# Performance work log

Hardware: AMD Instinct MI355X
Metric: run time of the kernel (lower is better)

The kernel has to match this reference:

```python
import jax, jax.numpy as jnp
import numpy as np

N_HEADS = 16
MAX_CACHE_LEN = 8192
LN_EPS = 1e-5


def _layernorm(x, g, b):
    mu = jnp.mean(x, axis=-1, keepdims=True)
    var = jnp.var(x, axis=-1, keepdims=True)
    return (x - mu) * jax.lax.rsqrt(var + LN_EPS) * g + b


def setup_inputs() -> dict:
    key = jax.random.key(0)
    ks = jax.random.split(key, 8)
    b, t, d, latdim, past = 2, 2048, 2048, 512, 2048
    s = 0.02
    return {
        "x": jax.random.normal(ks[0], (b, t, d), jnp.float32),
        "latent_prev": jax.random.normal(ks[1], (b, past, latdim), jnp.float32),
        "Wq": jax.random.normal(ks[2], (d, d), jnp.float32) * s,
        "Wdown": jax.random.normal(ks[3], (d, latdim), jnp.float32) * s,
        "Wk_up": jax.random.normal(ks[4], (latdim, d), jnp.float32) * s,
        "Wv_up": jax.random.normal(ks[5], (latdim, d), jnp.float32) * s,
        "ln_g": jnp.ones((latdim,), jnp.float32),
        "ln_b": jnp.zeros((latdim,), jnp.float32),
        "Wo": jax.random.normal(ks[6], (d, d), jnp.float32) * s,
    }


def reference(x, latent_prev, Wq, Wdown, Wk_up, Wv_up, ln_g, ln_b, Wo):
    b, t, d = x.shape
    H = N_HEADS
    hd = d // H
    # q projection -> [b, t, H, hd]
    q = (x @ Wq).reshape(b, t, H, hd)
    # latent down-projection + LayerNorm, concat with cache, trim to max_cache_len
    latent_new = _layernorm(x @ Wdown, ln_g, ln_b)
    latent = jnp.concatenate([latent_prev, latent_new], axis=1)
    latent = latent[:, -MAX_CACHE_LEN:]
    S = latent.shape[1]
    past_len = min(latent_prev.shape[1], S - t)
    # up-project K/V from latent -> [b, S, H, hd]
    k = (latent @ Wk_up).reshape(b, S, H, hd)
    v = (latent @ Wv_up).reshape(b, S, H, hd)
    # offset-causal SDPA: query i attends keys j <= past_len + i
    scores = jnp.einsum("bthd,bshd->bhts", q, k) / jnp.sqrt(jnp.asarray(hd, x.dtype))
    i = jnp.arange(t)[:, None]
    j = jnp.arange(S)[None, :]
    mask = j <= (past_len + i)  # [t, S]
    scores = jnp.where(mask[None, None], scores, jnp.asarray(-1e30, scores.dtype))
    attn = jax.nn.softmax(scores, axis=-1)
    out = jnp.einsum("bhts,bshd->bthd", attn, v).reshape(b, t, d)
    return out @ Wo
```

## Files before the change

kernel.cpp:

```cpp
#include <hip/hip_runtime.h>
#include <hip/hip_bf16.h>

using bf16_t = __bf16;
typedef __bf16 bf16x8 __attribute__((ext_vector_type(8)));
typedef __bf16 bf16x4 __attribute__((ext_vector_type(4)));
typedef __bf16 bf16x2 __attribute__((ext_vector_type(2)));
typedef float  f32x4  __attribute__((ext_vector_type(4)));
typedef float  f32x16 __attribute__((ext_vector_type(16)));
typedef unsigned u32x4 __attribute__((ext_vector_type(4)));

#define MFMA16(a,b,c) __builtin_amdgcn_mfma_f32_16x16x32_bf16((a),(b),(c),0,0,0)
#define MFMA32(a,b,c) __builtin_amdgcn_mfma_f32_32x32x16_bf16((a),(b),(c),0,0,0)

__device__ __forceinline__ void load_lds16(const void* g, void* l) {
  __builtin_amdgcn_global_load_lds(
      (const __attribute__((address_space(1))) unsigned int*)g,
      (__attribute__((address_space(3))) unsigned int*)l, 16, 0, 0);
}

__device__ __forceinline__ unsigned pack_bf16(float a, float b) {
  union { bf16x2 v; unsigned u; } c;
  c.v[0] = (bf16_t)a; c.v[1] = (bf16_t)b;
  return c.u;
}

__device__ __forceinline__ float fast_exp2(float x) {
#if __has_builtin(__builtin_amdgcn_exp2f)
  return __builtin_amdgcn_exp2f(x);
#else
  return exp2f(x);
#endif
}

__global__ __launch_bounds__(256) void cvt_f2b(const float* __restrict__ in,
                                               bf16_t* __restrict__ out)
{
  const size_t i = ((size_t)blockIdx.x * 256 + threadIdx.x) * 4;
  f32x4 d = *(const f32x4*)(in + i);
  bf16x4 o;
#pragma unroll
  for (int j = 0; j < 4; ++j) o[j] = (bf16_t)d[j];
  *(bf16x4*)(out + i) = o;
}

__global__ __launch_bounds__(256) void cvt_transpose(const float* __restrict__ in,
                                                     bf16_t* __restrict__ out,
                                                     int R, int C)
{
  __shared__ __align__(16) bf16_t t[64 * 80];
  const int r0 = blockIdx.y * 64, c0 = blockIdx.x * 64;
  const int rr = threadIdx.x >> 4;
  const int c4 = (threadIdx.x & 15) * 4;
#pragma unroll
  for (int i = 0; i < 4; ++i) {
    const int r = rr + i * 16;
    f32x4 d = *(const f32x4*)(in + (size_t)(r0 + r) * C + c0 + c4);
#pragma unroll
    for (int j = 0; j < 4; ++j) t[(c4 + j) * 80 + r] = (bf16_t)d[j];
  }
  __syncthreads();
  const int a  = threadIdx.x >> 3;
  const int bc = (threadIdx.x & 7) * 8;
#pragma unroll
  for (int half = 0; half < 2; ++half) {
    const int cc = a + half * 32;
    bf16x8 d = *(const bf16x8*)&t[cc * 80 + bc];
    *(bf16x8*)(out + (size_t)(c0 + cc) * R + r0 + bc) = d;
  }
}

template <typename OutT>
__global__ __launch_bounds__(256) void gemm128(const bf16_t* __restrict__ A,
                                               const bf16_t* __restrict__ BT,
                                               OutT* __restrict__ C,
                                               int M, int N, int K, float scale,
                                               long long zB, long long zC)
{
  __shared__ __align__(16) bf16_t As[128 * 32];
  __shared__ __align__(16) bf16_t Bs[128 * 32];
  const int tid = threadIdx.x;
  BT += (size_t)blockIdx.z * zB;
  C  += (size_t)blockIdx.z * zC;
  const int m0 = blockIdx.y * 128, n0 = blockIdx.x * 128;
  const int lane = tid & 63, w = tid >> 6;
  const int quad = lane >> 4, l15 = lane & 15;
  const int wm = (w >> 1) * 64, wn = (w & 1) * 64;
  const int s_row = tid >> 2;
  const int g_off = ((tid & 3) ^ (s_row & 3)) * 8;
  const int quadp = (quad ^ (l15 & 3)) * 8;
  const bf16_t* Ap0 = A  + (size_t)(m0 + s_row) * K + g_off;
  const bf16_t* Ap1 = A  + (size_t)(m0 + 64 + s_row) * K + g_off;
  const bf16_t* Bp0 = BT + (size_t)(n0 + s_row) * K + g_off;
  const bf16_t* Bp1 = BT + (size_t)(n0 + 64 + s_row) * K + g_off;

  f32x4 acc[4][4] = {};

  for (int k0 = 0; k0 < K; k0 += 32) {
    __syncthreads();
    load_lds16(Ap0 + k0, As + tid * 8);
    load_lds16(Ap1 + k0, As + tid * 8 + 2048);
    load_lds16(Bp0 + k0, Bs + tid * 8);
    load_lds16(Bp1 + k0, Bs + tid * 8 + 2048);
    __syncthreads();
    bf16x8 af[4], bfr[4];
#pragma unroll
    for (int fi = 0; fi < 4; ++fi)
      af[fi] = *(const bf16x8*)&As[(wm + fi * 16 + l15) * 32 + quadp];
#pragma unroll
    for (int fj = 0; fj < 4; ++fj)
      bfr[fj] = *(const bf16x8*)&Bs[(wn + fj * 16 + l15) * 32 + quadp];
#pragma unroll
    for (int fi = 0; fi < 4; ++fi)
#pragma unroll
      for (int fj = 0; fj < 4; ++fj)
        acc[fi][fj] = MFMA16(af[fi], bfr[fj], acc[fi][fj]);
  }

#pragma unroll
  for (int fi = 0; fi < 4; ++fi)
#pragma unroll
    for (int fj = 0; fj < 4; ++fj)
#pragma unroll
      for (int r = 0; r < 4; ++r) {
        const int row = m0 + wm + fi * 16 + quad * 4 + r;
        const int col = n0 + wn + fj * 16 + l15;
        C[(size_t)row * N + col] = (OutT)(acc[fi][fj][r] * scale);
      }
}

__global__ __launch_bounds__(256) void copy_prev_f(const float* __restrict__ prev,
                                                   bf16_t* __restrict__ latent)
{
  const size_t v    = (size_t)blockIdx.x * 256 + threadIdx.x;
  const size_t flat = v * 4;
  const size_t per  = (size_t)2048 * 512;
  const size_t b    = flat / per, rem = flat % per;
  f32x4 d = *(const f32x4*)(prev + flat);
  bf16x4 o;
#pragma unroll
  for (int j = 0; j < 4; ++j) o[j] = (bf16_t)d[j];
  *(bf16x4*)(latent + b * ((size_t)4096 * 512) + rem) = o;
}

__global__ __launch_bounds__(256) void ln_kernel(const bf16_t* __restrict__ in,
                                                 const float* __restrict__ g_,
                                                 const float* __restrict__ b_,
                                                 bf16_t* __restrict__ latent)
{
  const int row = blockIdx.x;
  const int tid = threadIdx.x;
  const float x0 = (float)in[(size_t)row * 512 + tid];
  const float x1 = (float)in[(size_t)row * 512 + 256 + tid];
  float s  = x0 + x1;
  float sq = x0 * x0 + x1 * x1;
#pragma unroll
  for (int off = 1; off < 64; off <<= 1) {
    s  += __shfl_xor(s, off);
    sq += __shfl_xor(sq, off);
  }
  __shared__ float red[8];
  const int w = tid >> 6;
  if ((tid & 63) == 0) { red[w] = s; red[4 + w] = sq; }
  __syncthreads();
  s  = red[0] + red[1] + red[2] + red[3];
  sq = red[4] + red[5] + red[6] + red[7];
  const float mu   = s * (1.0f / 512.0f);
  const float var  = sq * (1.0f / 512.0f) - mu * mu;
  const float rstd = rsqrtf(var + 1e-5f);
  const int b = row >> 11, tt = row & 2047;
  bf16_t* outp = latent + ((size_t)b * 4096 + 2048 + tt) * 512;
  outp[tid]       = (bf16_t)((x0 - mu) * rstd * g_[tid]       + b_[tid]);
  outp[tid + 256] = (bf16_t)((x1 - mu) * rstd * g_[tid + 256] + b_[tid + 256]);
}

__global__ __launch_bounds__(256) void attn7(const bf16_t* __restrict__ q,
                                             const bf16_t* __restrict__ k,
                                             const bf16_t* __restrict__ vT,
                                             bf16_t* __restrict__ out)
{
  __shared__ __align__(16) bf16_t smem[32768];

  const int tid = threadIdx.x;
  const int lane = tid & 63, w = tid >> 6;
  const int l31 = lane & 31, h5 = lane >> 5;

  const int g = blockIdx.x & 7, j = blockIdx.x >> 3;
  const int jl = j & 31, hsel = j >> 5;
  int qt = jl & 15;
  const int b = jl >> 4;
  if (hsel) qt = 15 - qt;
  const int h = g + 8 * hsel;

  const int q0 = qt * 128;
  const int qg = q0 + l31 * 4 + w;

  bf16x8 qf[8];
  const bf16_t* qb = q + ((size_t)(b * 2048 + qg)) * 2048 + h * 128 + h5 * 8;
#pragma unroll
  for (int fc = 0; fc < 8; ++fc) qf[fc] = *(const bf16x8*)(qb + fc * 16);

  const bf16_t* kbase = k + ((size_t)b * 4096) * 2048 + h * 128;
  const bf16_t* vbase = vT + ((size_t)(b * 16 + h)) * 128 * 4096;

  int ks_key[4], ks_go[4], vs_feat[4], vs_go[4];
#pragma unroll
  for (int p = 0; p < 4; ++p) {
    const int slot = tid + 256 * p;
    const int key = slot >> 4, ph = slot & 15;
    ks_key[p] = key;
    ks_go[p]  = (((ph & 8) | ((ph & 7) ^ (key & 7)))) * 8;
    const int ft = slot >> 3, p2 = slot & 7;
    vs_feat[p] = ft;
    vs_go[p]   = (p2 ^ (ft & 7)) * 8;
  }
  int kfo[8], vfo[4];
#pragma unroll
  for (int fc = 0; fc < 8; ++fc) {
    const int L = fc * 2 + h5;
    kfo[fc] = l31 * 128 + ((L & 8) | ((L & 7) ^ (l31 & 7))) * 8;
  }
#pragma unroll
  for (int kc = 0; kc < 4; ++kc) {
    const int L = kc * 2 + h5;
    vfo[kc] = l31 * 64 + (L ^ (l31 & 7)) * 8;
  }

  f32x16 o[4] = {};
  float m = -1e30f, l = 0.f;
  const int send = 2048 + q0 + 128;

#pragma unroll
  for (int p = 0; p < 4; ++p) {
    load_lds16(kbase + (size_t)ks_key[p] * 2048 + ks_go[p],
               smem + (tid + 256 * p) * 8);
    load_lds16(vbase + (size_t)vs_feat[p] * 4096 + vs_go[p],
               smem + 16384 + (tid + 256 * p) * 8);
  }
  __syncthreads();

  int cur = 0;
  for (int s0 = 0; s0 < send; s0 += 64) {
    const int s1 = s0 + 64;
    if (s1 < send) {
      const int nxt = (cur ^ 1) * 8192;
#pragma unroll
      for (int p = 0; p < 4; ++p) {
        load_lds16(kbase + (size_t)(s1 + ks_key[p]) * 2048 + ks_go[p],
                   smem + nxt + (tid + 256 * p) * 8);
        load_lds16(vbase + (size_t)vs_feat[p] * 4096 + s1 + vs_go[p],
                   smem + 16384 + nxt + (tid + 256 * p) * 8);
      }
    }
    const bf16_t* Kc = smem + cur * 8192;
    const bf16_t* Vc = smem + 16384 + cur * 8192;

    f32x16 st[2] = {};
    __builtin_amdgcn_s_setprio(1);
#pragma unroll
    for (int fc = 0; fc < 8; ++fc) {
      bf16x8 k0 = *(const bf16x8*)&Kc[kfo[fc]];
      bf16x8 k1 = *(const bf16x8*)&Kc[4096 + kfo[fc]];
      st[0] = MFMA32(k0, qf[fc], st[0]);
      st[1] = MFMA32(k1, qf[fc], st[1]);
    }
    __builtin_amdgcn_s_setprio(0);

    if (s0 + 63 > 2048 + q0) {
#pragma unroll
      for (int t = 0; t < 2; ++t)
#pragma unroll
        for (int i = 0; i < 16; ++i) {
          const int key = s0 + 32 * t + (i & 3) + 8 * (i >> 2) + 4 * h5;
          if (key > 2048 + qg) st[t][i] = -1e30f;
        }
    }

    float gm[8];
#pragma unroll
    for (int t = 0; t < 2; ++t)
#pragma unroll
      for (int gg = 0; gg < 4; ++gg)
        gm[t * 4 + gg] = fmaxf(fmaxf(st[t][4 * gg + 0], st[t][4 * gg + 1]),
                               fmaxf(st[t][4 * gg + 2], st[t][4 * gg + 3]));
    float mt = fmaxf(fmaxf(fmaxf(gm[0], gm[1]), fmaxf(gm[2], gm[3])),
                     fmaxf(fmaxf(gm[4], gm[5]), fmaxf(gm[6], gm[7])));
    mt = fmaxf(mt, __shfl_xor(mt, 32));

    if (__any(mt > m + 8.f)) {
      const float mnew = fmaxf(m, mt);
      const float alpha = fast_exp2(m - mnew);
#pragma unroll
      for (int ft = 0; ft < 4; ++ft)
#pragma unroll
        for (int i = 0; i < 16; ++i) o[ft][i] *= alpha;
      l *= alpha;
      m = mnew;
    }

    float rs = 0.f;
    unsigned up[2][4][2];
#pragma unroll
    for (int t = 0; t < 2; ++t)
#pragma unroll
      for (int gg = 0; gg < 4; ++gg) {
        const float p0 = fast_exp2(st[t][4 * gg + 0] - m);
        const float p1 = fast_exp2(st[t][4 * gg + 1] - m);
        const float p2 = fast_exp2(st[t][4 * gg + 2] - m);
        const float p3 = fast_exp2(st[t][4 * gg + 3] - m);
        rs += (p0 + p1) + (p2 + p3);
        up[t][gg][0] = pack_bf16(p0, p1);
        up[t][gg][1] = pack_bf16(p2, p3);
      }
    rs += __shfl_xor(rs, 32);
    l += rs;

#pragma unroll
    for (int kc = 0; kc < 4; ++kc) {
      const int t = kc >> 1, gp = (kc & 1) * 2;
      const unsigned a0 = up[t][gp][0],     a1 = up[t][gp][1];
      const unsigned b0 = up[t][gp + 1][0], b1 = up[t][gp + 1][1];
      const unsigned xa0 = __shfl_xor(a0, 32), xa1 = __shfl_xor(a1, 32);
      const unsigned xb0 = __shfl_xor(b0, 32), xb1 = __shfl_xor(b1, 32);
      u32x4 uw;
      uw[0] = h5 ? xb0 : a0;
      uw[1] = h5 ? xb1 : a1;
      uw[2] = h5 ? b0 : xa0;
      uw[3] = h5 ? b1 : xa1;
      union { u32x4 u; bf16x8 v; } pc; pc.u = uw;
      const bf16x8 pf = pc.v;
      __builtin_amdgcn_s_setprio(1);
#pragma unroll
      for (int ft = 0; ft < 4; ++ft) {
        bf16x8 vf = *(const bf16x8*)&Vc[ft * 2048 + vfo[kc]];
        o[ft] = MFMA32(vf, pf, o[ft]);
      }
      __builtin_amdgcn_s_setprio(0);
    }

    __syncthreads();
    cur ^= 1;
  }

  const float inv = 1.0f / l;
  const int rowp_w = w * 32 + l31;
#pragma unroll
  for (int ft = 0; ft < 4; ++ft)
#pragma unroll
    for (int gg = 0; gg < 4; ++gg) {
      bf16x4 pk;
#pragma unroll
      for (int r = 0; r < 4; ++r) pk[r] = (bf16_t)(o[ft][4 * gg + r] * inv);
      *(bf16x4*)&smem[rowp_w * 136 + ft * 32 + gg * 8 + h5 * 4] = pk;
    }
  __syncthreads();
#pragma unroll
  for (int p = 0; p < 8; ++p) {
    const int c = tid + 256 * p;
    const int rowp = c >> 4, chk = c & 15;
    const int ql = (rowp & 31) * 4 + (rowp >> 5);
    bf16x8 d = *(const bf16x8*)&smem[rowp * 136 + chk * 8];
    *(bf16x8*)(out + ((size_t)(b * 2048 + q0 + ql)) * 2048 + h * 128 + chk * 8) = d;
  }
}

extern "C" void kernel_launch(void* const* d_in, const int* in_sizes, int n_in,
                              void* d_out, int out_size, void* d_ws, size_t ws_size,
                              hipStream_t stream)
{
  (void)in_sizes; (void)n_in; (void)out_size; (void)ws_size;
  const float* x        = (const float*)d_in[0];
  const float* lat_prev = (const float*)d_in[1];
  const float* Wq       = (const float*)d_in[2];
  const float* Wdown    = (const float*)d_in[3];
  const float* Wk_up    = (const float*)d_in[4];
  const float* Wv_up    = (const float*)d_in[5];
  const float* ln_g     = (const float*)d_in[6];
  const float* ln_b     = (const float*)d_in[7];
  const float* Wo       = (const float*)d_in[8];
  float* out = (float*)d_out;

  char* p = (char*)d_ws;
  auto alloc = [&](size_t elems) { bf16_t* r = (bf16_t*)p; p += elems * 2; return r; };
  bf16_t* xb     = alloc((size_t)4096 * 2048);
  bf16_t* WqT    = alloc((size_t)2048 * 2048);
  bf16_t* WdT    = alloc((size_t)512 * 2048);
  bf16_t* qbuf   = alloc((size_t)4096 * 2048);
  bf16_t* latpre = alloc((size_t)4096 * 512);
  bf16_t* latent = alloc((size_t)2 * 4096 * 512);
  bf16_t* kbuf   = alloc((size_t)8192 * 2048);
  bf16_t* vTb    = alloc((size_t)2 * 2048 * 4096);
  bf16_t* aout   = alloc((size_t)4096 * 2048);
  bf16_t* WoT  = xb;
  bf16_t* WkT  = latpre;
  bf16_t* WvT  = latpre + (size_t)2048 * 512;

  const dim3 B(256);
  const float qscale = 0.12751744561825988f;

  cvt_f2b<<<dim3(8192), B, 0, stream>>>(x, xb);
  cvt_transpose<<<dim3(32, 32), B, 0, stream>>>(Wq,    WqT, 2048, 2048);
  cvt_transpose<<<dim3(8,  32), B, 0, stream>>>(Wdown, WdT, 2048, 512);
  gemm128<bf16_t><<<dim3(16, 32), B, 0, stream>>>(xb, WqT, qbuf, 4096, 2048, 2048, qscale, 0, 0);
  gemm128<bf16_t><<<dim3(4,  32), B, 0, stream>>>(xb, WdT, latpre, 4096, 512, 2048, 1.0f, 0, 0);
  copy_prev_f<<<dim3(2048), B, 0, stream>>>(lat_prev, latent);
  ln_kernel<<<dim3(4096), B, 0, stream>>>(latpre, ln_g, ln_b, latent);
  cvt_transpose<<<dim3(32, 32), B, 0, stream>>>(Wo,    WoT, 2048, 2048);
  cvt_transpose<<<dim3(32, 8),  B, 0, stream>>>(Wk_up, WkT, 512, 2048);
  cvt_transpose<<<dim3(32, 8),  B, 0, stream>>>(Wv_up, WvT, 512, 2048);
  gemm128<bf16_t><<<dim3(16, 64), B, 0, stream>>>(latent, WkT, kbuf, 8192, 2048, 512, 1.0f, 0, 0);
  gemm128<bf16_t><<<dim3(32, 16, 2), B, 0, stream>>>(WvT, latent, vTb, 2048, 4096, 512, 1.0f,
                                                     (long long)4096 * 512,
                                                     (long long)2048 * 4096);
  attn7<<<dim3(512), B, 0, stream>>>(qbuf, kbuf, vTb, aout);
  gemm128<float><<<dim3(16, 32), B, 0, stream>>>(aout, WoT, out, 4096, 2048, 2048, 1.0f, 0, 0);
}
```

Before: 578.7 us.

## Fuse Q and latent-down GEMMs into one launch and remap blocks across XCDs

Merges the x@Wq and x@Wdown projections into a single GEMM launch over a 2560-column output, splitting stores by column range into qbuf and latpre. This removes one launch and the tail underutilization of the small 128-block GEMM. It also adds an XCD-aware block-index remap to all 128x128 GEMMs so neighbouring tiles share an L2. The fused kernel assumes WdT sits immediately after WqT in the buffer allocation.

```diff
diff --git a/kernel.cpp b/kernel.cpp
--- a/kernel.cpp
+++ b/kernel.cpp
@@ -32,6 +32,19 @@
 #endif
 }
 
+__device__ __forceinline__ void xcd_remap(unsigned& bx, unsigned& by,
+                                          unsigned& bz)
+{
+  const unsigned nxy = gridDim.x * gridDim.y;
+  const unsigned nwg = nxy * gridDim.z;
+  unsigned wg = (blockIdx.z * gridDim.y + blockIdx.y) * gridDim.x + blockIdx.x;
+  if ((nwg & 7u) == 0u)
+    wg = (wg & 7u) * (nwg >> 3) + (wg >> 3);
+  bz = wg / nxy; wg -= bz * nxy;
+  by = wg / gridDim.x;
+  bx = wg - by * gridDim.x;
+}
+
 __global__ __launch_bounds__(256) void cvt_f2b(const float* __restrict__ in,
                                                bf16_t* __restrict__ out)
 {
@@ -79,9 +92,11 @@
   __shared__ __align__(16) bf16_t As[128 * 32];
   __shared__ __align__(16) bf16_t Bs[128 * 32];
   const int tid = threadIdx.x;
-  BT += (size_t)blockIdx.z * zB;
-  C  += (size_t)blockIdx.z * zC;
-  const int m0 = blockIdx.y * 128, n0 = blockIdx.x * 128;
+  unsigned bx, by, bz;
+  xcd_remap(bx, by, bz);
+  BT += (size_t)bz * zB;
+  C  += (size_t)bz * zC;
+  const int m0 = by * 128, n0 = bx * 128;
   const int lane = tid & 63, w = tid >> 6;
   const int quad = lane >> 4, l15 = lane & 15;
   const int wm = (w >> 1) * 64, wn = (w & 1) * 64;
@@ -125,6 +140,70 @@
         const int row = m0 + wm + fi * 16 + quad * 4 + r;
         const int col = n0 + wn + fj * 16 + l15;
         C[(size_t)row * N + col] = (OutT)(acc[fi][fj][r] * scale);
+      }
+}
+
+__global__ __launch_bounds__(256) void gemm128_dual(const bf16_t* __restrict__ A,
+                                                    const bf16_t* __restrict__ BT,
+                                                    bf16_t* __restrict__ C1,
+                                                    bf16_t* __restrict__ C2,
+                                                    float qscale)
+{
+  __shared__ __align__(16) bf16_t As[128 * 32];
+  __shared__ __align__(16) bf16_t Bs[128 * 32];
+  const int tid = threadIdx.x;
+  unsigned bx, by, bz;
+  xcd_remap(bx, by, bz);
+  const int K = 2048;
+  const int m0 = by * 128, n0 = bx * 128;
+  const int lane = tid & 63, w = tid >> 6;
+  const int quad = lane >> 4, l15 = lane & 15;
+  const int wm = (w >> 1) * 64, wn = (w & 1) * 64;
+  const int s_row = tid >> 2;
+  const int g_off = ((tid & 3) ^ (s_row & 3)) * 8;
+  const int quadp = (quad ^ (l15 & 3)) * 8;
+  const bf16_t* Ap0 = A  + (size_t)(m0 + s_row) * K + g_off;
+  const bf16_t* Ap1 = A  + (size_t)(m0 + 64 + s_row) * K + g_off;
+  const bf16_t* Bp0 = BT + (size_t)(n0 + s_row) * K + g_off;
+  const bf16_t* Bp1 = BT + (size_t)(n0 + 64 + s_row) * K + g_off;
+
+  f32x4 acc[4][4] = {};
+
+  for (int k0 = 0; k0 < K; k0 += 32) {
+    __syncthreads();
+    load_lds16(Ap0 + k0, As + tid * 8);
+    load_lds16(Ap1 + k0, As + tid * 8 + 2048);
+    load_lds16(Bp0 + k0, Bs + tid * 8);
+    load_lds16(Bp1 + k0, Bs + tid * 8 + 2048);
+    __syncthreads();
+    bf16x8 af[4], bfr[4];
+#pragma unroll
+    for (int fi = 0; fi < 4; ++fi)
+      af[fi] = *(const bf16x8*)&As[(wm + fi * 16 + l15) * 32 + quadp];
+#pragma unroll
+    for (int fj = 0; fj < 4; ++fj)
+      bfr[fj] = *(const bf16x8*)&Bs[(wn + fj * 16 + l15) * 32 + quadp];
+#pragma unroll
+    for (int fi = 0; fi < 4; ++fi)
+#pragma unroll
+      for (int fj = 0; fj < 4; ++fj)
+        acc[fi][fj] = MFMA16(af[fi], bfr[fj], acc[fi][fj]);
+  }
+
+  const bool isQ = (n0 < 2048);
+  const float sc = isQ ? qscale : 1.0f;
+#pragma unroll
+  for (int fi = 0; fi < 4; ++fi)
+#pragma unroll
+    for (int fj = 0; fj < 4; ++fj)
+#pragma unroll
+      for (int r = 0; r < 4; ++r) {
+        const int row = m0 + wm + fi * 16 + quad * 4 + r;
+        const int col = n0 + wn + fj * 16 + l15;
+        if (isQ)
+          C1[(size_t)row * 2048 + col] = (bf16_t)(acc[fi][fj][r] * sc);
+        else
+          C2[(size_t)row * 512 + (col - 2048)] = (bf16_t)(acc[fi][fj][r] * sc);
       }
 }
 
@@ -400,8 +479,7 @@
   cvt_f2b<<<dim3(8192), B, 0, stream>>>(x, xb);
   cvt_transpose<<<dim3(32, 32), B, 0, stream>>>(Wq,    WqT, 2048, 2048);
   cvt_transpose<<<dim3(8,  32), B, 0, stream>>>(Wdown, WdT, 2048, 512);
-  gemm128<bf16_t><<<dim3(16, 32), B, 0, stream>>>(xb, WqT, qbuf, 4096, 2048, 2048, qscale, 0, 0);
-  gemm128<bf16_t><<<dim3(4,  32), B, 0, stream>>>(xb, WdT, latpre, 4096, 512, 2048, 1.0f, 0, 0);
+  gemm128_dual<<<dim3(20, 32), B, 0, stream>>>(xb, WqT, qbuf, latpre, qscale);
   copy_prev_f<<<dim3(2048), B, 0, stream>>>(lat_prev, latent);
   ln_kernel<<<dim3(4096), B, 0, stream>>>(latpre, ln_g, ln_b, latent);
   cvt_transpose<<<dim3(32, 32), B, 0, stream>>>(Wo,    WoT, 2048, 2048);
```

Result: faster. 532.3 us (-8.0%).
